# Optimization experiments

Measured on AMD Instinct MI355X. Metric: run time of the kernel, lower is better.

The kernel has to match this reference:

```python
import jax, jax.numpy as jnp
import numpy as np

B, S_IMG, S_TXT, D, H, HD, R = 1, 1536, 512, 3072, 24, 128, 32
INNER = H * HD  # 3072
EPS = 1e-5


def svdq_linear(x, W, down, up, b=None):
    # Float reference of SVDQW4A4Linear: quantized base GEMM + SVD low-rank branch.
    y = x @ W.T + (x @ down) @ up
    if b is not None:
        y = y + b
    return y


def rms_norm(x, w):
    # RMSNorm over last dim (dim_head)
    var = jnp.mean(x * x, axis=-1, keepdims=True)
    return x * jax.lax.rsqrt(var + EPS) * w


def apply_rope(x, cos, sin):
    # x: (B, S, H, HD); cos/sin: (S, HD//2), interleaved complex rotation
    b, s, h, d = x.shape
    xr = x.reshape(b, s, h, d // 2, 2)
    x0, x1 = xr[..., 0], xr[..., 1]
    c = cos[None, :, None, :]
    sn = sin[None, :, None, :]
    o0 = x0 * c - x1 * sn
    o1 = x0 * sn + x1 * c
    return jnp.stack([o0, o1], axis=-1).reshape(b, s, h, d)


def setup_inputs() -> dict:
    key = jax.random.key(0)
    ks = jax.random.split(key, 24)
    sc = 0.02
    inp = {
        'hidden_states': jax.random.normal(ks[0], (B, S_IMG, D), jnp.float32),
        'encoder_hidden_states': jax.random.normal(ks[1], (B, S_TXT, D), jnp.float32),
    }
    S = S_IMG + S_TXT
    theta = jax.random.uniform(ks[2], (S, HD // 2), jnp.float32, 0.0, 2.0 * np.pi)
    inp['rope_cos'] = jnp.cos(theta)
    inp['rope_sin'] = jnp.sin(theta)
    inp['qkv_w'] = jax.random.normal(ks[3], (3 * INNER, D), jnp.float32) * sc
    inp['qkv_down'] = jax.random.normal(ks[4], (D, R), jnp.float32) * sc
    inp['qkv_up'] = jax.random.normal(ks[5], (R, 3 * INNER), jnp.float32) * sc
    inp['add_qkv_w'] = jax.random.normal(ks[6], (3 * INNER, D), jnp.float32) * sc
    inp['add_qkv_down'] = jax.random.normal(ks[7], (D, R), jnp.float32) * sc
    inp['add_qkv_up'] = jax.random.normal(ks[8], (R, 3 * INNER), jnp.float32) * sc
    inp['out_w'] = jax.random.normal(ks[9], (D, INNER), jnp.float32) * sc
    inp['out_down'] = jax.random.normal(ks[10], (INNER, R), jnp.float32) * sc
    inp['out_up'] = jax.random.normal(ks[11], (R, D), jnp.float32) * sc
    inp['out_b'] = jnp.zeros((D,), jnp.float32)
    inp['add_out_w'] = jax.random.normal(ks[12], (D, INNER), jnp.float32) * sc
    inp['add_out_down'] = jax.random.normal(ks[13], (INNER, R), jnp.float32) * sc
    inp['add_out_up'] = jax.random.normal(ks[14], (R, D), jnp.float32) * sc
    inp['add_out_b'] = jnp.zeros((D,), jnp.float32)
    inp['norm_q_w'] = jnp.ones((HD,), jnp.float32)
    inp['norm_k_w'] = jnp.ones((HD,), jnp.float32)
    inp['norm_added_q_w'] = jnp.ones((HD,), jnp.float32)
    inp['norm_added_k_w'] = jnp.ones((HD,), jnp.float32)
    return inp


def reference(hidden_states, encoder_hidden_states, rope_cos, rope_sin,
              qkv_w, qkv_down, qkv_up,
              add_qkv_w, add_qkv_down, add_qkv_up,
              out_w, out_down, out_up, out_b,
              add_out_w, add_out_down, add_out_up, add_out_b,
              norm_q_w, norm_k_w, norm_added_q_w, norm_added_k_w):
    seq_txt = encoder_hidden_states.shape[1]

    img_qkv = svdq_linear(hidden_states, qkv_w, qkv_down, qkv_up)
    img_q, img_k, img_v = jnp.split(img_qkv, 3, axis=-1)
    txt_qkv = svdq_linear(encoder_hidden_states, add_qkv_w, add_qkv_down, add_qkv_up)
    txt_q, txt_k, txt_v = jnp.split(txt_qkv, 3, axis=-1)

    def heads(x):
        return x.reshape(x.shape[0], x.shape[1], H, HD)

    img_q, img_k, img_v = heads(img_q), heads(img_k), heads(img_v)
    txt_q, txt_k, txt_v = heads(txt_q), heads(txt_k), heads(txt_v)

    img_q = rms_norm(img_q, norm_q_w)
    img_k = rms_norm(img_k, norm_k_w)
    txt_q = rms_norm(txt_q, norm_added_q_w)
    txt_k = rms_norm(txt_k, norm_added_k_w)

    q = jnp.concatenate([txt_q, img_q], axis=1)  # (B, S, H, HD)
    k = jnp.concatenate([txt_k, img_k], axis=1)
    v = jnp.concatenate([txt_v, img_v], axis=1)

    q = apply_rope(q, rope_cos, rope_sin)
    k = apply_rope(k, rope_cos, rope_sin)

    scale = 1.0 / jnp.sqrt(jnp.asarray(HD, q.dtype))
    scores = jnp.einsum('bqhd,bkhd->bhqk', q, k) * scale
    probs = jax.nn.softmax(scores, axis=-1)
    attn = jnp.einsum('bhqk,bkhd->bqhd', probs, v)
    attn = attn.reshape(attn.shape[0], attn.shape[1], INNER)

    txt_attn = attn[:, :seq_txt, :]
    img_attn = attn[:, seq_txt:, :]

    img_out = svdq_linear(img_attn, out_w, out_down, out_up, out_b)
    txt_out = svdq_linear(txt_attn, add_out_w, add_out_down, add_out_up, add_out_b)
    return (img_out, txt_out)
```

## Files before the change

kernel.cpp:

```cpp
#include <hip/hip_runtime.h>
#include <hip/hip_bf16.h>
#include <stdint.h>

typedef __hip_bfloat16 bf16;
typedef __attribute__((ext_vector_type(8))) short short8;
typedef __attribute__((ext_vector_type(4))) short short4b;
typedef __attribute__((ext_vector_type(4))) float floatx4;

__device__ __forceinline__ short bfs(float x) {
    uint32_t u = __builtin_bit_cast(uint32_t, x);
    u += 0x7FFFu + ((u >> 16) & 1u);
    return (short)(u >> 16);
}
__device__ __forceinline__ float b2f(bf16 x) { return __bfloat162float(x); }

__device__ __forceinline__ void load_lds16(const bf16* g, bf16* l) {
    __builtin_amdgcn_global_load_lds(
        (const __attribute__((address_space(1))) uint32_t*)g,
        (__attribute__((address_space(3))) uint32_t*)l, 16, 0, 0);
}

__global__ __launch_bounds__(256) void cvt_bf16(const float* __restrict__ X,
                                                bf16* __restrict__ Y) {
    const size_t i = ((size_t)blockIdx.x * 256 + threadIdx.x) * 8;
    const float4 v0 = *(const float4*)(X + i);
    const float4 v1 = *(const float4*)(X + i + 4);
    short8 o = { bfs(v0.x), bfs(v0.y), bfs(v0.z), bfs(v0.w),
                 bfs(v1.x), bfs(v1.y), bfs(v1.z), bfs(v1.w) };
    *(short8*)(Y + i) = o;
}

__global__ __launch_bounds__(64) void transposeR(const float* __restrict__ U,
                                                 bf16* __restrict__ UT, int N) {
    const int n = blockIdx.x * 64 + threadIdx.x;
    #pragma unroll
    for (int r = 0; r < 32; ++r)
        UT[(size_t)n * 32 + r] = __float2bfloat16(U[(size_t)r * N + n]);
}

__global__ __launch_bounds__(256) void downproj(const bf16* __restrict__ X,
                                                const float* __restrict__ Dn,
                                                bf16* __restrict__ T, int K) {
    const int m = blockIdx.x;
    const int n = threadIdx.x & 31;
    const int kg = threadIdx.x >> 5;
    const bf16* x = X + (size_t)m * K;
    const int kc = K >> 3;
    float acc = 0.f;
    #pragma unroll 4
    for (int k = kg * kc; k < (kg + 1) * kc; ++k)
        acc += b2f(x[k]) * Dn[(size_t)k * 32 + n];
    __shared__ float red[8][32];
    red[kg][n] = acc;
    __syncthreads();
    if (threadIdx.x < 32) {
        float s = 0.f;
        #pragma unroll
        for (int g = 0; g < 8; ++g) s += red[g][n];
        T[(size_t)m * 32 + n] = __float2bfloat16(s);
    }
}

__global__ __launch_bounds__(256) void gemm128(
    const bf16* __restrict__ A, const bf16* __restrict__ B,
    const bf16* __restrict__ T, const bf16* __restrict__ UpT,
    const float* __restrict__ bias, float* __restrict__ C,
    bf16* __restrict__ Qb, bf16* __restrict__ Kb, bf16* __restrict__ Vb,
    int M, int N, int K, int s_base, int mode)
{
    __shared__ __align__(16) bf16 As[128 * 32];
    __shared__ __align__(16) bf16 Bs[128 * 32];
    const int tid = threadIdx.x;
    const int lane = tid & 63, w = tid >> 6;
    const int wm = (w >> 1) * 64, wn = (w & 1) * 64;
    const int lr = lane & 15, lq = lane >> 4;

    int bid = blockIdx.y * gridDim.x + blockIdx.x;
    const int cpx = (gridDim.x * gridDim.y) >> 3;
    bid = (bid & 7) * cpx + (bid >> 3);
    const int by = bid / gridDim.x, bx = bid - by * gridDim.x;
    const int m0 = by * 128, n0 = bx * 128;

    floatx4 acc[4][4] = {};
    const int ksteps = K >> 5;
    for (int kt = 0; kt <= ksteps; ++kt) {
        const bf16 *a_src, *b_src;
        int lda, ldb;
        if (kt < ksteps) {
            a_src = A + (size_t)m0 * K + kt * 32; lda = K;
            b_src = B + (size_t)n0 * K + kt * 32; ldb = K;
        } else {
            a_src = T   + (size_t)m0 * 32; lda = 32;
            b_src = UpT + (size_t)n0 * 32; ldb = 32;
        }
        __syncthreads();
        #pragma unroll
        for (int it = 0; it < 2; ++it) {
            const int c = tid + it * 256;
            const int row = c >> 2, sub = c & 3;
            load_lds16(a_src + (size_t)row * lda + sub * 8, As + c * 8);
        }
        #pragma unroll
        for (int it = 0; it < 2; ++it) {
            const int c = tid + it * 256;
            const int row = c >> 2, sub = c & 3;
            load_lds16(b_src + (size_t)row * ldb + sub * 8, Bs + c * 8);
        }
        __syncthreads();
        short8 af[4], bfr[4];
        #pragma unroll
        for (int i = 0; i < 4; ++i)
            af[i] = *(const short8*)(As + (wm + i * 16 + lr) * 32 + lq * 8);
        #pragma unroll
        for (int j = 0; j < 4; ++j)
            bfr[j] = *(const short8*)(Bs + (wn + j * 16 + lr) * 32 + lq * 8);
        #pragma unroll
        for (int i = 0; i < 4; ++i)
            #pragma unroll
            for (int j = 0; j < 4; ++j)
                acc[i][j] = __builtin_amdgcn_mfma_f32_16x16x32_bf16(
                    af[i], bfr[j], acc[i][j], 0, 0, 0);
    }

    if (mode == 0) {
        #pragma unroll
        for (int j = 0; j < 4; ++j) {
            const int col = n0 + wn + j * 16 + lr;
            const float bv = bias ? bias[col] : 0.0f;
            #pragma unroll
            for (int i = 0; i < 4; ++i) {
                const int rowb = m0 + wm + i * 16 + lq * 4;
                #pragma unroll
                for (int r = 0; r < 4; ++r)
                    C[(size_t)(rowb + r) * N + col] = acc[i][j][r] + bv;
            }
        }
    } else {
        #pragma unroll
        for (int j = 0; j < 4; ++j) {
            const int col = n0 + wn + j * 16 + lr;
            const int which = col / 3072;
            const int cc = col - which * 3072;
            const int hh = cc >> 7, dd = cc & 127;
            #pragma unroll
            for (int i = 0; i < 4; ++i) {
                const int rowb = m0 + wm + i * 16 + lq * 4;
                #pragma unroll
                for (int r = 0; r < 4; ++r) {
                    const int s = s_base + rowb + r;
                    const bf16 v = __float2bfloat16(acc[i][j][r]);
                    if (which == 0)
                        Qb[((size_t)hh * 2048 + s) * 128 + dd] = v;
                    else if (which == 1)
                        Kb[((size_t)hh * 2048 + s) * 128 + dd] = v;
                    else
                        Vb[((size_t)hh * 128 + dd) * 2048 + s] = v;
                }
            }
        }
    }
}

__global__ __launch_bounds__(64) void rmsrope(
    bf16* __restrict__ Qb, bf16* __restrict__ Kb,
    const float* __restrict__ cosb, const float* __restrict__ sinb,
    const float* __restrict__ nqw, const float* __restrict__ nkw,
    const float* __restrict__ naqw, const float* __restrict__ nakw)
{
    const int s = blockIdx.x & 2047;
    const int h = blockIdx.x >> 11;
    const int i = threadIdx.x;
    const float c  = cosb[s * 64 + i];
    const float sn = sinb[s * 64 + i];
    const bool txt = (s < 512);
    const size_t base = ((size_t)h * 2048 + s) * 128;

    {
        __hip_bfloat162* row = (__hip_bfloat162*)(Qb + base);
        __hip_bfloat162 pv = row[i];
        float x0 = b2f(pv.x), x1 = b2f(pv.y);
        float ss = x0 * x0 + x1 * x1;
        #pragma unroll
        for (int m = 1; m < 64; m <<= 1) ss += __shfl_xor(ss, m);
        const float rms = rsqrtf(ss * (1.0f / 128.0f) + 1e-5f);
        const float* nw = txt ? naqw : nqw;
        const float y0 = x0 * rms * nw[2 * i];
        const float y1 = x1 * rms * nw[2 * i + 1];
        __hip_bfloat162 o;
        o.x = __float2bfloat16(y0 * c - y1 * sn);
        o.y = __float2bfloat16(y0 * sn + y1 * c);
        row[i] = o;
    }
    {
        __hip_bfloat162* row = (__hip_bfloat162*)(Kb + base);
        __hip_bfloat162 pv = row[i];
        float x0 = b2f(pv.x), x1 = b2f(pv.y);
        float ss = x0 * x0 + x1 * x1;
        #pragma unroll
        for (int m = 1; m < 64; m <<= 1) ss += __shfl_xor(ss, m);
        const float rms = rsqrtf(ss * (1.0f / 128.0f) + 1e-5f);
        const float* nw = txt ? nakw : nkw;
        const float y0 = x0 * rms * nw[2 * i];
        const float y1 = x1 * rms * nw[2 * i + 1];
        __hip_bfloat162 o;
        o.x = __float2bfloat16(y0 * c - y1 * sn);
        o.y = __float2bfloat16(y0 * sn + y1 * c);
        row[i] = o;
    }
}

__global__ __launch_bounds__(256) void attn64(
    const bf16* __restrict__ Qb, const bf16* __restrict__ Kb,
    const bf16* __restrict__ Vb, bf16* __restrict__ attnb)
{
    __shared__ __align__(16) bf16 Ks[64 * 128];
    __shared__ __align__(16) bf16 VsT[128 * 64];
    __shared__ __align__(16) bf16 Ps[4][16][72];
    const int tid = threadIdx.x, lane = tid & 63, w = tid >> 6;
    const int lr = lane & 15, lq = lane >> 4;
    const int h = blockIdx.y, q0 = blockIdx.x * 64;
    const float scale = 0.08838834764831845f;

    const bf16* qrow = Qb + ((size_t)h * 2048 + q0 + w * 16 + lr) * 128;
    short8 qf[4];
    #pragma unroll
    for (int ks = 0; ks < 4; ++ks)
        qf[ks] = *(const short8*)(qrow + ks * 32 + lq * 8);

    floatx4 oacc[8] = {};
    float mrow[4] = {-1e30f, -1e30f, -1e30f, -1e30f};
    float lrow[4] = {0.f, 0.f, 0.f, 0.f};

    for (int kt = 0; kt < 32; ++kt) {
        const int kv0 = kt * 64;
        __syncthreads();
        #pragma unroll
        for (int it = 0; it < 4; ++it) {
            const int c = tid + it * 256;
            const int row = c >> 4, cg = c & 15;
            load_lds16(Kb + ((size_t)h * 2048 + kv0 + row) * 128 + cg * 8,
                       Ks + c * 8);
        }
        #pragma unroll
        for (int it = 0; it < 4; ++it) {
            const int c = tid + it * 256;
            const int row = c >> 3, cg = c & 7;
            load_lds16(Vb + ((size_t)h * 128 + row) * 2048 + kv0 + cg * 8,
                       VsT + c * 8);
        }
        __syncthreads();

        floatx4 sacc[4] = {};
        #pragma unroll
        for (int ks = 0; ks < 4; ++ks)
            #pragma unroll
            for (int jt = 0; jt < 4; ++jt) {
                short8 kf = *(const short8*)(Ks + (jt * 16 + lr) * 128 + ks * 32 + lq * 8);
                sacc[jt] = __builtin_amdgcn_mfma_f32_16x16x32_bf16(qf[ks], kf, sacc[jt], 0, 0, 0);
            }

        float alpha_r[4];
        #pragma unroll
        for (int r = 0; r < 4; ++r) {
            float s0 = sacc[0][r] * scale, s1 = sacc[1][r] * scale;
            float s2 = sacc[2][r] * scale, s3 = sacc[3][r] * scale;
            float mx = fmaxf(fmaxf(s0, s1), fmaxf(s2, s3));
            #pragma unroll
            for (int msk = 1; msk < 16; msk <<= 1)
                mx = fmaxf(mx, __shfl_xor(mx, msk));
            const float mn = fmaxf(mrow[r], mx);
            const float al = __expf(mrow[r] - mn);
            s0 = __expf(s0 - mn); s1 = __expf(s1 - mn);
            s2 = __expf(s2 - mn); s3 = __expf(s3 - mn);
            float sum = s0 + s1 + s2 + s3;
            #pragma unroll
            for (int msk = 1; msk < 16; msk <<= 1)
                sum += __shfl_xor(sum, msk);
            lrow[r] = lrow[r] * al + sum;
            mrow[r] = mn;
            alpha_r[r] = al;
            sacc[0][r] = s0; sacc[1][r] = s1; sacc[2][r] = s2; sacc[3][r] = s3;
        }
        #pragma unroll
        for (int nt = 0; nt < 8; ++nt)
            #pragma unroll
            for (int r = 0; r < 4; ++r) oacc[nt][r] *= alpha_r[r];

        #pragma unroll
        for (int jt = 0; jt < 4; ++jt)
            #pragma unroll
            for (int r = 0; r < 4; ++r)
                Ps[w][lq * 4 + r][jt * 16 + lr] = __float2bfloat16(sacc[jt][r]);
        __syncthreads();

        short8 pf[2];
        #pragma unroll
        for (int k2 = 0; k2 < 2; ++k2)
            pf[k2] = *(const short8*)(&Ps[w][lr][k2 * 32 + lq * 8]);
        #pragma unroll
        for (int k2 = 0; k2 < 2; ++k2)
            #pragma unroll
            for (int nt = 0; nt < 8; ++nt) {
                short8 vf = *(const short8*)(VsT + (nt * 16 + lr) * 64 + k2 * 32 + lq * 8);
                oacc[nt] = __builtin_amdgcn_mfma_f32_16x16x32_bf16(pf[k2], vf, oacc[nt], 0, 0, 0);
            }
    }

    #pragma unroll
    for (int nt = 0; nt < 8; ++nt) {
        const int col = h * 128 + nt * 16 + lr;
        #pragma unroll
        for (int r = 0; r < 4; ++r) {
            const int s = q0 + w * 16 + lq * 4 + r;
            attnb[(size_t)s * 3072 + col] = __float2bfloat16(oacc[nt][r] / lrow[r]);
        }
    }
}

extern "C" void kernel_launch(void* const* d_in, const int* in_sizes, int n_in,
                              void* d_out, int out_size, void* d_ws, size_t ws_size,
                              hipStream_t stream)
{
    (void)in_sizes; (void)n_in; (void)out_size; (void)ws_size;
    const float* hs        = (const float*)d_in[0];
    const float* ehs       = (const float*)d_in[1];
    const float* rc        = (const float*)d_in[2];
    const float* rs        = (const float*)d_in[3];
    const float* qkv_w     = (const float*)d_in[4];
    const float* qkv_down  = (const float*)d_in[5];
    const float* qkv_up    = (const float*)d_in[6];
    const float* aqkv_w    = (const float*)d_in[7];
    const float* aqkv_down = (const float*)d_in[8];
    const float* aqkv_up   = (const float*)d_in[9];
    const float* out_w     = (const float*)d_in[10];
    const float* out_down  = (const float*)d_in[11];
    const float* out_up    = (const float*)d_in[12];
    const float* out_b     = (const float*)d_in[13];
    const float* aout_w    = (const float*)d_in[14];
    const float* aout_down = (const float*)d_in[15];
    const float* aout_up   = (const float*)d_in[16];
    const float* aout_b    = (const float*)d_in[17];
    const float* nqw  = (const float*)d_in[18];
    const float* nkw  = (const float*)d_in[19];
    const float* naqw = (const float*)d_in[20];
    const float* nakw = (const float*)d_in[21];

    char* ws = (char*)d_ws;
    size_t o = 0;
    bf16* Qb = (bf16*)(ws + o); o += (size_t)24 * 2048 * 128 * 2;
    bf16* Kb = (bf16*)(ws + o); o += (size_t)24 * 2048 * 128 * 2;
    bf16* Vb = (bf16*)(ws + o); o += (size_t)24 * 2048 * 128 * 2;
    bf16* attnb = (bf16*)(ws + o); o += (size_t)2048 * 3072 * 2;
    bf16* Xbi = (bf16*)(ws + o); o += (size_t)1536 * 3072 * 2;
    bf16* Xbt = (bf16*)(ws + o); o += (size_t)512 * 3072 * 2;
    bf16* Wq  = (bf16*)(ws + o); o += (size_t)9216 * 3072 * 2;
    bf16* Waq = (bf16*)(ws + o); o += (size_t)9216 * 3072 * 2;
    bf16* Wo  = Wq;
    bf16* Wao = Wq + (size_t)3072 * 3072;
    bf16* t_img  = (bf16*)(ws + o); o += (size_t)1536 * 32 * 2;
    bf16* t_txt  = (bf16*)(ws + o); o += (size_t)512 * 32 * 2;
    bf16* t2_img = (bf16*)(ws + o); o += (size_t)1536 * 32 * 2;
    bf16* t2_txt = (bf16*)(ws + o); o += (size_t)512 * 32 * 2;
    bf16* upTq  = (bf16*)(ws + o); o += (size_t)9216 * 32 * 2;
    bf16* upTaq = (bf16*)(ws + o); o += (size_t)9216 * 32 * 2;
    bf16* upTo  = (bf16*)(ws + o); o += (size_t)3072 * 32 * 2;
    bf16* upTao = (bf16*)(ws + o); o += (size_t)3072 * 32 * 2;

    cvt_bf16<<<2304, 256, 0, stream>>>(hs, Xbi);
    cvt_bf16<<<768, 256, 0, stream>>>(ehs, Xbt);
    cvt_bf16<<<13824, 256, 0, stream>>>(qkv_w, Wq);
    cvt_bf16<<<13824, 256, 0, stream>>>(aqkv_w, Waq);

    transposeR<<<144, 64, 0, stream>>>(qkv_up, upTq, 9216);
    transposeR<<<144, 64, 0, stream>>>(aqkv_up, upTaq, 9216);
    transposeR<<<48, 64, 0, stream>>>(out_up, upTo, 3072);
    transposeR<<<48, 64, 0, stream>>>(aout_up, upTao, 3072);
    downproj<<<1536, 256, 0, stream>>>(Xbi, qkv_down, t_img, 3072);
    downproj<<<512, 256, 0, stream>>>(Xbt, aqkv_down, t_txt, 3072);

    gemm128<<<dim3(72, 12), 256, 0, stream>>>(Xbi, Wq, t_img, upTq,
        nullptr, nullptr, Qb, Kb, Vb, 1536, 9216, 3072, 512, 1);
    gemm128<<<dim3(72, 4), 256, 0, stream>>>(Xbt, Waq, t_txt, upTaq,
        nullptr, nullptr, Qb, Kb, Vb, 512, 9216, 3072, 0, 1);

    cvt_bf16<<<4608, 256, 0, stream>>>(out_w, Wo);
    cvt_bf16<<<4608, 256, 0, stream>>>(aout_w, Wao);

    rmsrope<<<24 * 2048, 64, 0, stream>>>(Qb, Kb, rc, rs, nqw, nkw, naqw, nakw);

    attn64<<<dim3(32, 24), 256, 0, stream>>>(Qb, Kb, Vb, attnb);

    downproj<<<1536, 256, 0, stream>>>(attnb + (size_t)512 * 3072, out_down, t2_img, 3072);
    downproj<<<512, 256, 0, stream>>>(attnb, aout_down, t2_txt, 3072);

    float* outp = (float*)d_out;
    gemm128<<<dim3(24, 12), 256, 0, stream>>>(attnb + (size_t)512 * 3072, Wo,
        t2_img, upTo, out_b, outp, nullptr, nullptr, nullptr,
        1536, 3072, 3072, 0, 0);
    gemm128<<<dim3(24, 4), 256, 0, stream>>>(attnb, Wao,
        t2_txt, upTao, aout_b, outp + (size_t)1536 * 3072, nullptr, nullptr, nullptr,
        512, 3072, 3072, 0, 0);
}
```

Measured before the change: 1.170 ms.

## Swizzle attention LDS tiles, drop P-tile barrier, vectorize V stores, set MFMA priority

The K, V^T and P shared-memory tiles in the attention kernel switch to an XOR-swizzled layout, which removes LDS bank conflicts on the 16-byte MFMA operand reads. The block-wide barrier between the P write and read is dropped because each wave only touches its own P slice. The QKV GEMM epilogue writes V^T as 4-element vector stores, MFMA sections get s_setprio, and the final normalization multiplies by a reciprocal. The swizzle must match exactly between the global_load_lds writes and the reads, and dropping the barrier relies on the wave's own LDS ordering being enough.

```diff
diff --git a/kernel.cpp b/kernel.cpp
--- a/kernel.cpp
+++ b/kernel.cpp
@@ -145,16 +145,17 @@
             #pragma unroll
             for (int i = 0; i < 4; ++i) {
                 const int rowb = m0 + wm + i * 16 + lq * 4;
-                #pragma unroll
-                for (int r = 0; r < 4; ++r) {
-                    const int s = s_base + rowb + r;
-                    const bf16 v = __float2bfloat16(acc[i][j][r]);
-                    if (which == 0)
-                        Qb[((size_t)hh * 2048 + s) * 128 + dd] = v;
-                    else if (which == 1)
-                        Kb[((size_t)hh * 2048 + s) * 128 + dd] = v;
-                    else
-                        Vb[((size_t)hh * 128 + dd) * 2048 + s] = v;
+                const int s0 = s_base + rowb;
+                if (which == 2) {
+                    short4b pv = { bfs(acc[i][j][0]), bfs(acc[i][j][1]),
+                                   bfs(acc[i][j][2]), bfs(acc[i][j][3]) };
+                    *(short4b*)(Vb + ((size_t)hh * 128 + dd) * 2048 + s0) = pv;
+                } else {
+                    bf16* dst = (which == 0 ? Qb : Kb)
+                              + ((size_t)hh * 2048 + s0) * 128 + dd;
+                    #pragma unroll
+                    for (int r = 0; r < 4; ++r)
+                        dst[(size_t)r * 128] = __float2bfloat16(acc[i][j][r]);
                 }
             }
         }
@@ -215,7 +216,7 @@
 {
     __shared__ __align__(16) bf16 Ks[64 * 128];
     __shared__ __align__(16) bf16 VsT[128 * 64];
-    __shared__ __align__(16) bf16 Ps[4][16][72];
+    __shared__ __align__(16) bf16 Ps[4][16 * 64];
     const int tid = threadIdx.x, lane = tid & 63, w = tid >> 6;
     const int lr = lane & 15, lq = lane >> 4;
     const int h = blockIdx.y, q0 = blockIdx.x * 64;
@@ -237,27 +238,31 @@
         #pragma unroll
         for (int it = 0; it < 4; ++it) {
             const int c = tid + it * 256;
-            const int row = c >> 4, cg = c & 15;
+            const int row = c >> 4, cg = (c & 15) ^ (row & 7);
             load_lds16(Kb + ((size_t)h * 2048 + kv0 + row) * 128 + cg * 8,
                        Ks + c * 8);
         }
         #pragma unroll
         for (int it = 0; it < 4; ++it) {
             const int c = tid + it * 256;
-            const int row = c >> 3, cg = c & 7;
+            const int row = c >> 3, cg = (c & 7) ^ (row & 7);
             load_lds16(Vb + ((size_t)h * 128 + row) * 2048 + kv0 + cg * 8,
                        VsT + c * 8);
         }
         __syncthreads();
 
         floatx4 sacc[4] = {};
+        __builtin_amdgcn_s_setprio(1);
         #pragma unroll
         for (int ks = 0; ks < 4; ++ks)
             #pragma unroll
             for (int jt = 0; jt < 4; ++jt) {
-                short8 kf = *(const short8*)(Ks + (jt * 16 + lr) * 128 + ks * 32 + lq * 8);
+                const int row = jt * 16 + lr;
+                short8 kf = *(const short8*)(
+                    Ks + row * 128 + (((ks * 4 + lq) ^ (row & 7)) * 8));
                 sacc[jt] = __builtin_amdgcn_mfma_f32_16x16x32_bf16(qf[ks], kf, sacc[jt], 0, 0, 0);
             }
+        __builtin_amdgcn_s_setprio(0);
 
         float alpha_r[4];
         #pragma unroll
@@ -289,30 +294,41 @@
         #pragma unroll
         for (int jt = 0; jt < 4; ++jt)
             #pragma unroll
-            for (int r = 0; r < 4; ++r)
-                Ps[w][lq * 4 + r][jt * 16 + lr] = __float2bfloat16(sacc[jt][r]);
-        __syncthreads();
+            for (int r = 0; r < 4; ++r) {
+                const int q = lq * 4 + r;
+                const int ir = jt * 16 + lr;
+                Ps[w][q * 64 + ((((ir >> 3) ^ (q & 7))) << 3) + (ir & 7)] =
+                    __float2bfloat16(sacc[jt][r]);
+            }
 
         short8 pf[2];
         #pragma unroll
         for (int k2 = 0; k2 < 2; ++k2)
-            pf[k2] = *(const short8*)(&Ps[w][lr][k2 * 32 + lq * 8]);
+            pf[k2] = *(const short8*)(
+                &Ps[w][lr * 64 + (((k2 * 4 + lq) ^ (lr & 7)) << 3)]);
+        __builtin_amdgcn_s_setprio(1);
         #pragma unroll
         for (int k2 = 0; k2 < 2; ++k2)
             #pragma unroll
             for (int nt = 0; nt < 8; ++nt) {
-                short8 vf = *(const short8*)(VsT + (nt * 16 + lr) * 64 + k2 * 32 + lq * 8);
+                const int row = nt * 16 + lr;
+                short8 vf = *(const short8*)(
+                    VsT + row * 64 + (((k2 * 4 + lq) ^ (row & 7)) * 8));
                 oacc[nt] = __builtin_amdgcn_mfma_f32_16x16x32_bf16(pf[k2], vf, oacc[nt], 0, 0, 0);
             }
-    }
-
+        __builtin_amdgcn_s_setprio(0);
+    }
+
+    float rl[4];
+    #pragma unroll
+    for (int r = 0; r < 4; ++r) rl[r] = 1.0f / lrow[r];
     #pragma unroll
     for (int nt = 0; nt < 8; ++nt) {
         const int col = h * 128 + nt * 16 + lr;
         #pragma unroll
         for (int r = 0; r < 4; ++r) {
             const int s = q0 + w * 16 + lq * 4 + r;
-            attnb[(size_t)s * 3072 + col] = __float2bfloat16(oacc[nt][r] / lrow[r]);
+            attnb[(size_t)s * 3072 + col] = __float2bfloat16(oacc[nt][r] * rl[r]);
         }
     }
 }
```

Result: faster. 1.104 ms (-5.6%).
